# Kernel optimization log

Hardware: AMD Instinct MI355X
Metric: run time of the kernel (lower is better)

## Reference

```python
import jax, jax.numpy as jnp
import numpy as np

T = 2048
HIDDEN = 4096
NQ = 32
NKV = 8
HD = 128
THETA = 10000.0


def setup_inputs() -> dict:
    key = jax.random.key(0)
    ks = jax.random.split(key, 5)
    s = 1.0 / np.sqrt(HIDDEN)
    return {
        "positions": jnp.arange(T, dtype=jnp.int32),
        "hidden_states": jax.random.normal(ks[0], (T, HIDDEN), dtype=jnp.float32),
        "wq": jax.random.normal(ks[1], (HIDDEN, NQ * HD), dtype=jnp.float32) * s,
        "wk": jax.random.normal(ks[2], (HIDDEN, NKV * HD), dtype=jnp.float32) * s,
        "wv": jax.random.normal(ks[3], (HIDDEN, NKV * HD), dtype=jnp.float32) * s,
        "wo": jax.random.normal(ks[4], (NQ * HD, HIDDEN), dtype=jnp.float32) * s,
    }


def _rope_neox(x, positions):
    # x: [T, H, HD]; neox style: split halves, rotate
    half = HD // 2
    inv_freq = 1.0 / (THETA ** (jnp.arange(0, half, dtype=jnp.float32) / half))
    ang = positions.astype(jnp.float32)[:, None] * inv_freq[None, :]  # [T, half]
    cos = jnp.cos(ang)[:, None, :]  # [T, 1, half]
    sin = jnp.sin(ang)[:, None, :]
    x1, x2 = x[..., :half], x[..., half:]
    return jnp.concatenate([x1 * cos - x2 * sin, x2 * cos + x1 * sin], axis=-1)


def reference(positions, hidden_states, wq, wk, wv, wo):
    scale = HD ** -0.5
    q = (hidden_states @ wq).reshape(T, NQ, HD)
    k = (hidden_states @ wk).reshape(T, NKV, HD)
    v = (hidden_states @ wv).reshape(T, NKV, HD)
    q = _rope_neox(q, positions)
    k = _rope_neox(k, positions)
    # GQA: repeat kv heads to match q heads
    group = NQ // NKV
    k_r = jnp.repeat(k, group, axis=1)  # [T, NQ, HD]
    v_r = jnp.repeat(v, group, axis=1)
    scores = jnp.einsum('qhd,khd->hqk', q, k_r) * scale  # [NQ, T, T]
    causal = positions[:, None] >= positions[None, :]  # [T, T]
    scores = jnp.where(causal[None, :, :], scores, -jnp.inf)
    probs = jax.nn.softmax(scores, axis=-1)
    attn = jnp.einsum('hqk,khd->qhd', probs, v_r).reshape(T, NQ * HD)
    return attn @ wo
```

## Files before the change

### kernel.cpp

```cpp
#include <hip/hip_runtime.h>

#define T_SEQ  2048
#define HID    4096
#define NQH    32
#define NKVH   8
#define HDIM   128

typedef float  f32x4  __attribute__((ext_vector_type(4)));
typedef __bf16 bf16x8 __attribute__((ext_vector_type(8)));

__device__ __forceinline__ float bf2f(unsigned short u) {
  union { unsigned int i; float f; } v; v.i = ((unsigned int)u) << 16; return v.f;
}
__device__ __forceinline__ unsigned short f2bf(float f) {
  union { float f; unsigned int i; } v; v.f = f;
  unsigned int r = v.i + 0x7fffu + ((v.i >> 16) & 1u);
  return (unsigned short)(r >> 16);
}

__device__ __forceinline__ f32x4 mfma_bf16(bf16x8 a, bf16x8 b, f32x4 c) {
  return __builtin_amdgcn_mfma_f32_16x16x32_bf16(a, b, c, 0, 0, 0);
}

#define GLOAD16(g, l)                                              \
  __builtin_amdgcn_global_load_lds(                                \
      (const __attribute__((address_space(1))) void*)(g),          \
      (__attribute__((address_space(3))) void*)(l), 16, 0, 0)

__global__ void prep_all(const float* __restrict__ hs, unsigned short* __restrict__ hb,
                         const float* __restrict__ wq, unsigned short* __restrict__ wqt,
                         const float* __restrict__ wk, const float* __restrict__ wv,
                         unsigned short* __restrict__ wkvt) {
  __shared__ float tile[64][65];
  const int b = blockIdx.x;
  if (b < 8192) {
    long long i = ((long long)b * 256 + threadIdx.x) * 4;
    float4 v = *(const float4*)(hs + i);
    union { unsigned short u[4]; uint2 p; } o;
    o.u[0] = f2bf(v.x); o.u[1] = f2bf(v.y); o.u[2] = f2bf(v.z); o.u[3] = f2bf(v.w);
    *(uint2*)(hb + i) = o.p;
    return;
  }
  const float* W;
  unsigned short* dst;
  int N, n0, k0;
  if (b < 12288) {
    int bid = b - 8192;  W = wq;  dst = wqt;  N = 4096;
    n0 = (bid & 63) * 64; k0 = (bid >> 6) * 64;
  } else if (b < 13312) {
    int bid = b - 12288; W = wk;  dst = wkvt; N = 1024;
    n0 = (bid & 15) * 64; k0 = (bid >> 4) * 64;
  } else {
    int bid = b - 13312; W = wv;  dst = wkvt + (size_t)1024 * HID; N = 1024;
    n0 = (bid & 15) * 64; k0 = (bid >> 4) * 64;
  }
  int tx = threadIdx.x & 15, ty = threadIdx.x >> 4;
#pragma unroll
  for (int i = 0; i < 4; i++) {
    int k = ty + 16 * i;
    float4 f = *(const float4*)(W + (long long)(k0 + k) * N + n0 + tx * 4);
    tile[tx * 4 + 0][k] = f.x;
    tile[tx * 4 + 1][k] = f.y;
    tile[tx * 4 + 2][k] = f.z;
    tile[tx * 4 + 3][k] = f.w;
  }
  __syncthreads();
#pragma unroll
  for (int i = 0; i < 4; i++) {
    int n = ty + 16 * i;
    union { unsigned short u[4]; uint2 p; } o;
    o.u[0] = f2bf(tile[n][tx * 4 + 0]);
    o.u[1] = f2bf(tile[n][tx * 4 + 1]);
    o.u[2] = f2bf(tile[n][tx * 4 + 2]);
    o.u[3] = f2bf(tile[n][tx * 4 + 3]);
    *(uint2*)(dst + (long long)(n0 + n) * HID + k0 + tx * 4) = o.p;
  }
}

__global__ void transpose_conv(const float* __restrict__ W,
                               unsigned short* __restrict__ Wt, int K, int N) {
  __shared__ float tile[64][65];
  int n0 = blockIdx.x * 64, k0 = blockIdx.y * 64;
  int tx = threadIdx.x & 15, ty = threadIdx.x >> 4;
#pragma unroll
  for (int i = 0; i < 4; i++) {
    int k = ty + 16 * i;
    float4 f = *(const float4*)(W + (long long)(k0 + k) * N + n0 + tx * 4);
    tile[tx * 4 + 0][k] = f.x;
    tile[tx * 4 + 1][k] = f.y;
    tile[tx * 4 + 2][k] = f.z;
    tile[tx * 4 + 3][k] = f.w;
  }
  __syncthreads();
#pragma unroll
  for (int i = 0; i < 4; i++) {
    int n = ty + 16 * i;
    union { unsigned short u[4]; uint2 p; } o;
    o.u[0] = f2bf(tile[n][tx * 4 + 0]);
    o.u[1] = f2bf(tile[n][tx * 4 + 1]);
    o.u[2] = f2bf(tile[n][tx * 4 + 2]);
    o.u[3] = f2bf(tile[n][tx * 4 + 3]);
    *(uint2*)(Wt + (long long)(n0 + n) * K + k0 + tx * 4) = o.p;
  }
}

template <int EPI>
__global__ __launch_bounds__(256) void gemm_bt(const unsigned short* __restrict__ A,
                                               const unsigned short* __restrict__ Bt,
                                               void* __restrict__ Cv,
                                               int M, int N, int K) {
  __shared__ unsigned short As[128 * 64];
  __shared__ unsigned short Bs[128 * 64];
  const int lin = blockIdx.y * gridDim.x + blockIdx.x;
  const int cpx = (gridDim.x * gridDim.y) >> 3;
  const int swz = (lin & 7) * cpx + (lin >> 3);
  const int bx = swz % gridDim.x, by = swz / gridDim.x;

  const int t = threadIdx.x;
  const int lane = t & 63, w = t >> 6;
  const int wr = w >> 1, wc = w & 1;
  const int l15 = lane & 15, lg = lane >> 4;
  const int m0 = by * 128, n0 = bx * 128;

  f32x4 acc[4][4];
#pragma unroll
  for (int i = 0; i < 4; i++)
#pragma unroll
    for (int j = 0; j < 4; j++) acc[i][j] = (f32x4){0.f, 0.f, 0.f, 0.f};

  for (int kt = 0; kt < K; kt += 64) {
    __syncthreads();
#pragma unroll
    for (int s = 0; s < 4; s++) {
      int c = t + s * 256;
      int row = c >> 3, sub = c & 7;
      GLOAD16(A + (long long)(m0 + row) * K + kt + ((sub ^ (row & 7)) * 8),
              (char*)As + (w * 64 + s * 256) * 16);
      GLOAD16(Bt + (long long)(n0 + row) * K + kt + ((sub ^ (row & 7)) * 8),
              (char*)Bs + (w * 64 + s * 256) * 16);
    }
    __syncthreads();

#pragma unroll
    for (int kk = 0; kk < 2; kk++) {
      bf16x8 af[4], bfr[4];
#pragma unroll
      for (int mi = 0; mi < 4; mi++) {
        int row = wr * 64 + mi * 16 + l15;
        af[mi] = *(const bf16x8*)(As + row * 64 + (((kk * 4 + lg) ^ (row & 7)) * 8));
      }
#pragma unroll
      for (int ni = 0; ni < 4; ni++) {
        int row = wc * 64 + ni * 16 + l15;
        bfr[ni] = *(const bf16x8*)(Bs + row * 64 + (((kk * 4 + lg) ^ (row & 7)) * 8));
      }
#pragma unroll
      for (int mi = 0; mi < 4; mi++)
#pragma unroll
        for (int ni = 0; ni < 4; ni++)
          acc[mi][ni] = mfma_bf16(af[mi], bfr[ni], acc[mi][ni]);
    }
  }

  const int row0 = m0 + wr * 64, col0 = n0 + wc * 64;
#pragma unroll
  for (int mi = 0; mi < 4; mi++)
#pragma unroll
    for (int ni = 0; ni < 4; ni++) {
      int rbase = row0 + mi * 16 + lg * 4;
      int col = col0 + ni * 16 + l15;
#pragma unroll
      for (int r = 0; r < 4; r++) {
        float v = acc[mi][ni][r];
        if (EPI == 0)
          ((unsigned short*)Cv)[(long long)(rbase + r) * N + col] = f2bf(v);
        else
          ((float*)Cv)[(long long)(rbase + r) * N + col] = v;
      }
    }
}

__global__ __launch_bounds__(256) void gemm_qkv(const unsigned short* __restrict__ A,
                                                const unsigned short* __restrict__ wqt,
                                                const unsigned short* __restrict__ wkvt,
                                                unsigned short* __restrict__ qb,
                                                unsigned short* __restrict__ kb,
                                                unsigned short* __restrict__ vtb) {
  __shared__ unsigned short S[2 * 128 * 64];
  unsigned short* As = S;
  unsigned short* Bs = S + 128 * 64;
  const int K = HID;

  const int lin = blockIdx.y * gridDim.x + blockIdx.x;
  const int cpx = (gridDim.x * gridDim.y) >> 3;
  const int swz = (lin & 7) * cpx + (lin >> 3);
  const int bx = swz % gridDim.x, by = swz / gridDim.x;

  const int t = threadIdx.x;
  const int lane = t & 63, w = t >> 6;
  const int wr = w >> 1, wc = w & 1;
  const int l15 = lane & 15, lg = lane >> 4;
  const int m0 = by * 128, n0 = bx * 128;

  const unsigned short* Brow = (n0 < 4096) ? (wqt + (long long)n0 * K)
                                           : (wkvt + (long long)(n0 - 4096) * K);

  f32x4 acc[4][4];
#pragma unroll
  for (int i = 0; i < 4; i++)
#pragma unroll
    for (int j = 0; j < 4; j++) acc[i][j] = (f32x4){0.f, 0.f, 0.f, 0.f};

  for (int kt = 0; kt < K; kt += 64) {
    __syncthreads();
#pragma unroll
    for (int s = 0; s < 4; s++) {
      int c = t + s * 256;
      int row = c >> 3, sub = c & 7;
      GLOAD16(A + (long long)(m0 + row) * K + kt + ((sub ^ (row & 7)) * 8),
              (char*)As + (w * 64 + s * 256) * 16);
      GLOAD16(Brow + (long long)row * K + kt + ((sub ^ (row & 7)) * 8),
              (char*)Bs + (w * 64 + s * 256) * 16);
    }
    __syncthreads();

#pragma unroll
    for (int kk = 0; kk < 2; kk++) {
      bf16x8 af[4], bfr[4];
#pragma unroll
      for (int mi = 0; mi < 4; mi++) {
        int row = wr * 64 + mi * 16 + l15;
        af[mi] = *(const bf16x8*)(As + row * 64 + (((kk * 4 + lg) ^ (row & 7)) * 8));
      }
#pragma unroll
      for (int ni = 0; ni < 4; ni++) {
        int row = wc * 64 + ni * 16 + l15;
        bfr[ni] = *(const bf16x8*)(Bs + row * 64 + (((kk * 4 + lg) ^ (row & 7)) * 8));
      }
#pragma unroll
      for (int mi = 0; mi < 4; mi++)
#pragma unroll
        for (int ni = 0; ni < 4; ni++)
          acc[mi][ni] = mfma_bf16(af[mi], bfr[ni], acc[mi][ni]);
    }
  }

  const int row0 = m0 + wr * 64;
  if (n0 < 4096) {
#pragma unroll
    for (int mi = 0; mi < 4; mi++)
#pragma unroll
      for (int ni = 0; ni < 4; ni++) {
        int rbase = row0 + mi * 16 + lg * 4;
        int col = n0 + wc * 64 + ni * 16 + l15;
#pragma unroll
        for (int r = 0; r < 4; r++)
          qb[(long long)(rbase + r) * 4096 + col] = f2bf(acc[mi][ni][r]);
      }
  } else if (n0 < 5120) {
#pragma unroll
    for (int mi = 0; mi < 4; mi++)
#pragma unroll
      for (int ni = 0; ni < 4; ni++) {
        int rbase = row0 + mi * 16 + lg * 4;
        int col = (n0 - 4096) + wc * 64 + ni * 16 + l15;
#pragma unroll
        for (int r = 0; r < 4; r++)
          kb[(long long)(rbase + r) * 1024 + col] = f2bf(acc[mi][ni][r]);
      }
  } else {
    __syncthreads();
    unsigned short* Tt = S;
#pragma unroll
    for (int mi = 0; mi < 4; mi++)
#pragma unroll
      for (int ni = 0; ni < 4; ni++) {
        int nloc = wc * 64 + ni * 16 + l15;
#pragma unroll
        for (int r = 0; r < 4; r++) {
          int mloc = wr * 64 + mi * 16 + lg * 4 + r;
          Tt[nloc * 128 + (mloc & 64) + ((mloc & 63) ^ ((nloc & 7) << 3))] =
              f2bf(acc[mi][ni][r]);
        }
      }
    __syncthreads();
    const int nloc = t >> 1;
    const int half = t & 1;
    const int d0 = n0 - 5120;
#pragma unroll
    for (int ci = 0; ci < 16; ci++) {
      uint2 v = *(const uint2*)(Tt + nloc * 128 + half * 64 +
                                (((ci >> 1) ^ (nloc & 7)) * 8 + (ci & 1) * 4));
      int nc = (ci >> 3) * 8 + 2 * (ci & 3) + ((ci >> 2) & 1);
      *(uint2*)(vtb + (long long)(d0 + nloc) * T_SEQ + m0 + half * 64 + nc * 4) = v;
    }
  }
}

__global__ void rope_all(unsigned short* __restrict__ qb,
                         unsigned short* __restrict__ kb,
                         const int* __restrict__ positions,
                         int* __restrict__ cnt) {
  if (blockIdx.x == 0 && threadIdx.x < 8) cnt[threadIdx.x] = 0;
  const int w = threadIdx.x >> 6, d = threadIdx.x & 63;
  const int gid = blockIdx.x * 4 + w;
  unsigned short* row;
  int t;
  bool isq;
  if (gid < T_SEQ * NQH) {
    int h = gid & (NQH - 1); t = gid >> 5;
    row = qb + (size_t)t * (NQH * HDIM) + (size_t)h * HDIM;
    isq = true;
  } else {
    int g = gid - T_SEQ * NQH;
    int h = g & (NKVH - 1); t = g >> 3;
    row = kb + (size_t)t * (NKVH * HDIM) + (size_t)h * HDIM;
    isq = false;
  }
  double inv = exp2(-(double)d * 0.20762050593046014);
  double ang = (double)positions[t] * inv;
  double c = cos(ang), s = sin(ang);
  if (isq) { c *= 0.12751744416986895; s *= 0.12751744416986895; }
  float x1 = bf2f(row[d]), x2 = bf2f(row[d + 64]);
  row[d]      = f2bf((float)((double)x1 * c - (double)x2 * s));
  row[d + 64] = f2bf((float)((double)x2 * c + (double)x1 * s));
}

__global__ __launch_bounds__(256) void attn_kernel(const unsigned short* __restrict__ qb,
                                                   const unsigned short* __restrict__ kb,
                                                   const unsigned short* __restrict__ vt,
                                                   unsigned short* __restrict__ ab,
                                                   int* __restrict__ cnt) {
  __shared__ unsigned short Ks[64 * 128];
  __shared__ unsigned short Vs[128 * 64];
  __shared__ int s_item;

  const int xcd = blockIdx.x & 7;
  const int kvh = xcd;
  const int t = threadIdx.x, lane = t & 63, w = t >> 6;
  const int l15 = lane & 15, lg = lane >> 4;

  for (;;) {
    __syncthreads();
    if (t == 0) s_item = atomicAdd(&cnt[xcd], 1);
    __syncthreads();
    const int item = s_item;
    if (item >= 128) break;
    const int j = 31 - (item >> 2);
    const int head = xcd * 4 + (item & 3);
    const int q0 = j * 64;

    bf16x8 qf[4];
#pragma unroll
    for (int kk = 0; kk < 4; kk++)
      qf[kk] = *(const bf16x8*)(qb + (long long)(q0 + w * 16 + l15) * (NQH * HDIM) +
                                head * HDIM + kk * 32 + lg * 8);

    f32x4 accO[8];
#pragma unroll
    for (int db = 0; db < 8; db++) accO[db] = (f32x4){0.f, 0.f, 0.f, 0.f};
    float mrun = -3e38f, lrun = 0.f;

    for (int kt = 0; kt <= j; kt++) {
      __syncthreads();
#pragma unroll
      for (int s = 0; s < 4; s++) {
        int c = t + s * 256;
        int row = c >> 4, chk = c & 15;
        GLOAD16(kb + (long long)(kt * 64 + row) * (NKVH * HDIM) + kvh * HDIM +
                    ((chk ^ (row & 7)) * 8),
                (char*)Ks + (w * 64 + s * 256) * 16);
      }
#pragma unroll
      for (int s = 0; s < 4; s++) {
        int c = t + s * 256;
        int row = c >> 3, chk = c & 7;
        GLOAD16(vt + (long long)(kvh * HDIM + row) * T_SEQ + kt * 64 +
                    ((chk ^ (row & 7)) * 8),
                (char*)Vs + (w * 64 + s * 256) * 16);
      }
      __syncthreads();

      f32x4 accS[4];
#pragma unroll
      for (int kc = 0; kc < 4; kc++) accS[kc] = (f32x4){0.f, 0.f, 0.f, 0.f};
      __builtin_amdgcn_s_setprio(1);
#pragma unroll
      for (int kk = 0; kk < 4; kk++)
#pragma unroll
        for (int kc = 0; kc < 4; kc++) {
          int row = kc * 16 + l15;
          bf16x8 a = *(const bf16x8*)(Ks + row * 128 + (((kk * 4 + lg) ^ (l15 & 7)) * 8));
          accS[kc] = mfma_bf16(a, qf[kk], accS[kc]);
        }
      __builtin_amdgcn_s_setprio(0);

      float pm[4][4];
      if (kt == j) {
        const int qloc = w * 16 + l15;
#pragma unroll
        for (int kc = 0; kc < 4; kc++)
#pragma unroll
          for (int r = 0; r < 4; r++)
            pm[kc][r] = (kc * 16 + lg * 4 + r > qloc) ? -3e38f : accS[kc][r];
      } else {
#pragma unroll
        for (int kc = 0; kc < 4; kc++)
#pragma unroll
          for (int r = 0; r < 4; r++) pm[kc][r] = accS[kc][r];
      }

      float rm = pm[0][0];
#pragma unroll
      for (int kc = 0; kc < 4; kc++)
#pragma unroll
        for (int r = 0; r < 4; r++) rm = fmaxf(rm, pm[kc][r]);
      if (__any(rm > mrun + 8.f)) {
        rm = fmaxf(rm, __shfl_xor(rm, 16, 64));
        rm = fmaxf(rm, __shfl_xor(rm, 32, 64));
        float mn = fmaxf(mrun, rm);
        float corr = exp2f(mrun - mn);
        mrun = mn;
        lrun *= corr;
        float cO[4];
#pragma unroll
        for (int r = 0; r < 4; r++) cO[r] = __shfl(corr, lg * 4 + r, 64);
#pragma unroll
        for (int db = 0; db < 8; db++)
#pragma unroll
          for (int r = 0; r < 4; r++) accO[db][r] *= cO[r];
      }

      float p[4][4];
#pragma unroll
      for (int kc = 0; kc < 4; kc++)
#pragma unroll
        for (int r = 0; r < 4; r++) {
          p[kc][r] = exp2f(pm[kc][r] - mrun);
          lrun += p[kc][r];
        }
      bf16x8 pa0, pa1;
#pragma unroll
      for (int jj = 0; jj < 8; jj++) {
        pa0[jj] = (__bf16)p[(jj >> 2)][jj & 3];
        pa1[jj] = (__bf16)p[2 + (jj >> 2)][jj & 3];
      }

      __builtin_amdgcn_s_setprio(1);
#pragma unroll
      for (int db = 0; db < 8; db++) {
        int vrow = db * 16 + l15;
        bf16x8 b = *(const bf16x8*)(Vs + vrow * 64 + ((lg ^ (vrow & 7)) * 8));
        accO[db] = mfma_bf16(pa0, b, accO[db]);
      }
#pragma unroll
      for (int db = 0; db < 8; db++) {
        int vrow = db * 16 + l15;
        bf16x8 b = *(const bf16x8*)(Vs + vrow * 64 + (((4 + lg) ^ (vrow & 7)) * 8));
        accO[db] = mfma_bf16(pa1, b, accO[db]);
      }
      __builtin_amdgcn_s_setprio(0);
    }

    lrun += __shfl_xor(lrun, 16, 64);
    lrun += __shfl_xor(lrun, 32, 64);
    float lO[4];
#pragma unroll
    for (int r = 0; r < 4; r++) lO[r] = __shfl(lrun, lg * 4 + r, 64);
#pragma unroll
    for (int db = 0; db < 8; db++)
#pragma unroll
      for (int r = 0; r < 4; r++) {
        int qr = q0 + w * 16 + lg * 4 + r;
        int col = head * HDIM + db * 16 + l15;
        ((__bf16*)ab)[(long long)qr * (NQH * HDIM) + col] = (__bf16)(accO[db][r] / lO[r]);
      }
  }
}

extern "C" void kernel_launch(void* const* d_in, const int* in_sizes, int n_in,
                              void* d_out, int out_size, void* d_ws, size_t ws_size,
                              hipStream_t stream) {
  const int*   positions = (const int*)d_in[0];
  const float* hs = (const float*)d_in[1];
  const float* wq = (const float*)d_in[2];
  const float* wk = (const float*)d_in[3];
  const float* wv = (const float*)d_in[4];
  const float* wo = (const float*)d_in[5];
  float* out = (float*)d_out;

  const size_t SZ_WQT = (size_t)HID * HID * 2;
  const size_t SZ_WKV = (size_t)2048 * HID * 2;
  const size_t SZ_HB  = (size_t)T_SEQ * HID * 2;
  const size_t SZ_QB  = (size_t)T_SEQ * NQH * HDIM * 2;
  const size_t SZ_KB  = (size_t)T_SEQ * NKVH * HDIM * 2;
  const size_t need = SZ_WQT + SZ_WKV + SZ_HB + SZ_QB + SZ_KB * 2 + 64;
  if (ws_size < need) return;

  char* p = (char*)d_ws;
  unsigned short* wqt  = (unsigned short*)p; p += SZ_WQT;
  unsigned short* wkvt = (unsigned short*)p; p += SZ_WKV;
  unsigned short* hb   = (unsigned short*)p; p += SZ_HB;
  unsigned short* qb   = (unsigned short*)p; p += SZ_QB;
  unsigned short* kb   = (unsigned short*)p; p += SZ_KB;
  unsigned short* vtb  = (unsigned short*)p; p += SZ_KB;
  int* cnt = (int*)p;
  unsigned short* ab   = hb;

  prep_all<<<14336, 256, 0, stream>>>(hs, hb, wq, wqt, wk, wv, wkvt);

  gemm_qkv<<<dim3(48, 16), 256, 0, stream>>>(hb, wqt, wkvt, qb, kb, vtb);

  rope_all<<<(T_SEQ * (NQH + NKVH)) / 4, 256, 0, stream>>>(qb, kb, positions, cnt);

  attn_kernel<<<512, 256, 0, stream>>>(qb, kb, vtb, ab, cnt);

  transpose_conv<<<dim3(HID / 64, (NQH * HDIM) / 64), 256, 0, stream>>>(wo, wqt, NQH * HDIM, HID);
  gemm_bt<2><<<dim3(HID / 128, T_SEQ / 128), 256, 0, stream>>>(ab, wqt, out, T_SEQ, HID, NQH * HDIM);
}
```

Baseline: 384.1 us.

## Split QKV GEMM into Q and KV tile types to balance grid

The fused QKV GEMM grid goes from 768 uniform 128x128 tiles to 1024 blocks. Blocks alternate in groups of eight between Q tiles (128x128) and K/V tiles that use a smaller 64x128 M tile. The aim is more blocks and a better wave fill across the GPU's compute units, with Q and KV work interleaved. The cost is that the smaller KV tiles reuse data less per block, and the V transpose epilogue is adapted to 64-row tiles.

New measurement: 384.4 us. Within noise of the previous version (+0.1%).

```diff
diff --git a/kernel.cpp b/kernel.cpp
--- a/kernel.cpp
+++ b/kernel.cpp
@@ -180,119 +180,168 @@
     }
 }
 
-__global__ __launch_bounds__(256) void gemm_qkv(const unsigned short* __restrict__ A,
-                                                const unsigned short* __restrict__ wqt,
-                                                const unsigned short* __restrict__ wkvt,
-                                                unsigned short* __restrict__ qb,
-                                                unsigned short* __restrict__ kb,
-                                                unsigned short* __restrict__ vtb) {
+__global__ __launch_bounds__(256) void gemm_qkv2(const unsigned short* __restrict__ A,
+                                                 const unsigned short* __restrict__ wqt,
+                                                 const unsigned short* __restrict__ wkvt,
+                                                 unsigned short* __restrict__ qb,
+                                                 unsigned short* __restrict__ kb,
+                                                 unsigned short* __restrict__ vtb) {
   __shared__ unsigned short S[2 * 128 * 64];
   unsigned short* As = S;
   unsigned short* Bs = S + 128 * 64;
   const int K = HID;
 
-  const int lin = blockIdx.y * gridDim.x + blockIdx.x;
-  const int cpx = (gridDim.x * gridDim.y) >> 3;
-  const int swz = (lin & 7) * cpx + (lin >> 3);
-  const int bx = swz % gridDim.x, by = swz / gridDim.x;
+  const int b = blockIdx.x;
+  const int type = (b >> 3) & 1;
+  const int id = ((b >> 4) << 3) | (b & 7);
 
   const int t = threadIdx.x;
   const int lane = t & 63, w = t >> 6;
   const int wr = w >> 1, wc = w & 1;
   const int l15 = lane & 15, lg = lane >> 4;
-  const int m0 = by * 128, n0 = bx * 128;
-
-  const unsigned short* Brow = (n0 < 4096) ? (wqt + (long long)n0 * K)
-                                           : (wkvt + (long long)(n0 - 4096) * K);
-
-  f32x4 acc[4][4];
-#pragma unroll
-  for (int i = 0; i < 4; i++)
-#pragma unroll
-    for (int j = 0; j < 4; j++) acc[i][j] = (f32x4){0.f, 0.f, 0.f, 0.f};
-
-  for (int kt = 0; kt < K; kt += 64) {
-    __syncthreads();
-#pragma unroll
-    for (int s = 0; s < 4; s++) {
-      int c = t + s * 256;
-      int row = c >> 3, sub = c & 7;
-      GLOAD16(A + (long long)(m0 + row) * K + kt + ((sub ^ (row & 7)) * 8),
-              (char*)As + (w * 64 + s * 256) * 16);
-      GLOAD16(Brow + (long long)row * K + kt + ((sub ^ (row & 7)) * 8),
-              (char*)Bs + (w * 64 + s * 256) * 16);
-    }
-    __syncthreads();
-
-#pragma unroll
-    for (int kk = 0; kk < 2; kk++) {
-      bf16x8 af[4], bfr[4];
-#pragma unroll
-      for (int mi = 0; mi < 4; mi++) {
-        int row = wr * 64 + mi * 16 + l15;
-        af[mi] = *(const bf16x8*)(As + row * 64 + (((kk * 4 + lg) ^ (row & 7)) * 8));
-      }
-#pragma unroll
-      for (int ni = 0; ni < 4; ni++) {
-        int row = wc * 64 + ni * 16 + l15;
-        bfr[ni] = *(const bf16x8*)(Bs + row * 64 + (((kk * 4 + lg) ^ (row & 7)) * 8));
-      }
-#pragma unroll
-      for (int mi = 0; mi < 4; mi++)
-#pragma unroll
-        for (int ni = 0; ni < 4; ni++)
-          acc[mi][ni] = mfma_bf16(af[mi], bfr[ni], acc[mi][ni]);
-    }
-  }
-
-  const int row0 = m0 + wr * 64;
-  if (n0 < 4096) {
+
+  if (type == 0) {
+    const int swz = (id & 7) * 64 + (id >> 3);
+    const int bx = swz & 31, by = swz >> 5;
+    const int m0 = by * 128, n0 = bx * 128;
+
+    f32x4 acc[4][4];
+#pragma unroll
+    for (int i = 0; i < 4; i++)
+#pragma unroll
+      for (int j = 0; j < 4; j++) acc[i][j] = (f32x4){0.f, 0.f, 0.f, 0.f};
+
+    for (int kt = 0; kt < K; kt += 64) {
+      __syncthreads();
+#pragma unroll
+      for (int s = 0; s < 4; s++) {
+        int c = t + s * 256;
+        int row = c >> 3, sub = c & 7;
+        GLOAD16(A + (long long)(m0 + row) * K + kt + ((sub ^ (row & 7)) * 8),
+                (char*)As + (w * 64 + s * 256) * 16);
+        GLOAD16(wqt + (long long)(n0 + row) * K + kt + ((sub ^ (row & 7)) * 8),
+                (char*)Bs + (w * 64 + s * 256) * 16);
+      }
+      __syncthreads();
+
+#pragma unroll
+      for (int kk = 0; kk < 2; kk++) {
+        bf16x8 af[4], bfr[4];
+#pragma unroll
+        for (int mi = 0; mi < 4; mi++) {
+          int row = wr * 64 + mi * 16 + l15;
+          af[mi] = *(const bf16x8*)(As + row * 64 + (((kk * 4 + lg) ^ (row & 7)) * 8));
+        }
+#pragma unroll
+        for (int ni = 0; ni < 4; ni++) {
+          int row = wc * 64 + ni * 16 + l15;
+          bfr[ni] = *(const bf16x8*)(Bs + row * 64 + (((kk * 4 + lg) ^ (row & 7)) * 8));
+        }
+#pragma unroll
+        for (int mi = 0; mi < 4; mi++)
+#pragma unroll
+          for (int ni = 0; ni < 4; ni++)
+            acc[mi][ni] = mfma_bf16(af[mi], bfr[ni], acc[mi][ni]);
+      }
+    }
+
+    const int row0 = m0 + wr * 64, col0 = n0 + wc * 64;
 #pragma unroll
     for (int mi = 0; mi < 4; mi++)
 #pragma unroll
       for (int ni = 0; ni < 4; ni++) {
         int rbase = row0 + mi * 16 + lg * 4;
-        int col = n0 + wc * 64 + ni * 16 + l15;
+        int col = col0 + ni * 16 + l15;
 #pragma unroll
         for (int r = 0; r < 4; r++)
-          qb[(long long)(rbase + r) * 4096 + col] = f2bf(acc[mi][ni][r]);
-      }
-  } else if (n0 < 5120) {
-#pragma unroll
-    for (int mi = 0; mi < 4; mi++)
-#pragma unroll
-      for (int ni = 0; ni < 4; ni++) {
-        int rbase = row0 + mi * 16 + lg * 4;
-        int col = (n0 - 4096) + wc * 64 + ni * 16 + l15;
-#pragma unroll
-        for (int r = 0; r < 4; r++)
-          kb[(long long)(rbase + r) * 1024 + col] = f2bf(acc[mi][ni][r]);
+          qb[(long long)(rbase + r) * (NQH * HDIM) + col] = f2bf(acc[mi][ni][r]);
       }
   } else {
-    __syncthreads();
-    unsigned short* Tt = S;
-#pragma unroll
-    for (int mi = 0; mi < 4; mi++)
-#pragma unroll
-      for (int ni = 0; ni < 4; ni++) {
-        int nloc = wc * 64 + ni * 16 + l15;
-#pragma unroll
-        for (int r = 0; r < 4; r++) {
-          int mloc = wr * 64 + mi * 16 + lg * 4 + r;
-          Tt[nloc * 128 + (mloc & 64) + ((mloc & 63) ^ ((nloc & 7) << 3))] =
-              f2bf(acc[mi][ni][r]);
-        }
-      }
-    __syncthreads();
-    const int nloc = t >> 1;
-    const int half = t & 1;
-    const int d0 = n0 - 5120;
-#pragma unroll
-    for (int ci = 0; ci < 16; ci++) {
-      uint2 v = *(const uint2*)(Tt + nloc * 128 + half * 64 +
-                                (((ci >> 1) ^ (nloc & 7)) * 8 + (ci & 1) * 4));
-      int nc = (ci >> 3) * 8 + 2 * (ci & 3) + ((ci >> 2) & 1);
-      *(uint2*)(vtb + (long long)(d0 + nloc) * T_SEQ + m0 + half * 64 + nc * 4) = v;
+    const int swz = (id & 7) * 64 + (id >> 3);
+    const int bx = swz & 15, by = swz >> 4;
+    const int m0 = by * 64, n0 = bx * 128;
+
+    f32x4 acc[2][4];
+#pragma unroll
+    for (int i = 0; i < 2; i++)
+#pragma unroll
+      for (int j = 0; j < 4; j++) acc[i][j] = (f32x4){0.f, 0.f, 0.f, 0.f};
+
+    for (int kt = 0; kt < K; kt += 64) {
+      __syncthreads();
+#pragma unroll
+      for (int s = 0; s < 2; s++) {
+        int c = t + s * 256;
+        int row = c >> 3, sub = c & 7;
+        GLOAD16(A + (long long)(m0 + row) * K + kt + ((sub ^ (row & 7)) * 8),
+                (char*)As + (w * 64 + s * 256) * 16);
+      }
+#pragma unroll
+      for (int s = 0; s < 4; s++) {
+        int c = t + s * 256;
+        int row = c >> 3, sub = c & 7;
+        GLOAD16(wkvt + (long long)(n0 + row) * K + kt + ((sub ^ (row & 7)) * 8),
+                (char*)Bs + (w * 64 + s * 256) * 16);
+      }
+      __syncthreads();
+
+#pragma unroll
+      for (int kk = 0; kk < 2; kk++) {
+        bf16x8 af[2], bfr[4];
+#pragma unroll
+        for (int mi = 0; mi < 2; mi++) {
+          int row = wr * 32 + mi * 16 + l15;
+          af[mi] = *(const bf16x8*)(As + row * 64 + (((kk * 4 + lg) ^ (row & 7)) * 8));
+        }
+#pragma unroll
+        for (int ni = 0; ni < 4; ni++) {
+          int row = wc * 64 + ni * 16 + l15;
+          bfr[ni] = *(const bf16x8*)(Bs + row * 64 + (((kk * 4 + lg) ^ (row & 7)) * 8));
+        }
+#pragma unroll
+        for (int mi = 0; mi < 2; mi++)
+#pragma unroll
+          for (int ni = 0; ni < 4; ni++)
+            acc[mi][ni] = mfma_bf16(af[mi], bfr[ni], acc[mi][ni]);
+      }
+    }
+
+    const int row0 = m0 + wr * 32, col0 = n0 + wc * 64;
+    if (n0 < 1024) {
+#pragma unroll
+      for (int mi = 0; mi < 2; mi++)
+#pragma unroll
+        for (int ni = 0; ni < 4; ni++) {
+          int rbase = row0 + mi * 16 + lg * 4;
+          int col = col0 + ni * 16 + l15;
+#pragma unroll
+          for (int r = 0; r < 4; r++)
+            kb[(long long)(rbase + r) * 1024 + col] = f2bf(acc[mi][ni][r]);
+        }
+    } else {
+      __syncthreads();
+      unsigned short* Tt = S;
+#pragma unroll
+      for (int mi = 0; mi < 2; mi++)
+#pragma unroll
+        for (int ni = 0; ni < 4; ni++) {
+          int nloc = wc * 64 + ni * 16 + l15;
+#pragma unroll
+          for (int r = 0; r < 4; r++) {
+            int mloc = wr * 32 + mi * 16 + lg * 4 + r;
+            Tt[nloc * 64 + (mloc ^ ((nloc & 7) << 3))] = f2bf(acc[mi][ni][r]);
+          }
+        }
+      __syncthreads();
+      const int nloc = t >> 1;
+#pragma unroll
+      for (int cc = 0; cc < 8; cc++) {
+        int ci = (t & 1) * 8 + cc;
+        uint2 v = *(const uint2*)(Tt + nloc * 64 +
+                                  (((ci >> 1) ^ (nloc & 7)) * 8 + (ci & 1) * 4));
+        int nc = (ci >> 3) * 8 + 2 * (ci & 3) + ((ci >> 2) & 1);
+        *(uint2*)(vtb + (long long)(n0 - 1024 + nloc) * T_SEQ + m0 + nc * 4) = v;
+      }
     }
   }
 }
@@ -509,7 +558,7 @@
 
   prep_all<<<14336, 256, 0, stream>>>(hs, hb, wq, wqt, wk, wv, wkvt);
 
-  gemm_qkv<<<dim3(48, 16), 256, 0, stream>>>(hb, wqt, wkvt, qb, kb, vtb);
+  gemm_qkv2<<<1024, 256, 0, stream>>>(hb, wqt, wkvt, qb, kb, vtb);
 
   rope_all<<<(T_SEQ * (NQH + NKVH)) / 4, 256, 0, stream>>>(qb, kb, positions, cnt);
 
```

## Double-buffer attention K/V tiles and split QKV GEMM into Q and KV kernels

Applied to the files above, without the earlier changes.

The attention kernel now keeps two shared-memory buffers for K and V. It prefetches the next key tile while computing on the current one, so global loads overlap MFMA work instead of sitting behind a barrier. The fused QKV projection is replaced by the generic gemm_bt for Q plus a new 64x128-tile KV GEMM. The smaller KV tiles give more blocks for the narrow K/V output. In exchange, attention shared memory doubles, which may lower occupancy, and the extra launch adds a little overhead.

New measurement: 357.5 us (median of 2 runs). 1.07x faster.

```diff
diff --git a/kernel.cpp b/kernel.cpp
--- a/kernel.cpp
+++ b/kernel.cpp
@@ -180,56 +180,54 @@
     }
 }
 
-__global__ __launch_bounds__(256) void gemm_qkv(const unsigned short* __restrict__ A,
-                                                const unsigned short* __restrict__ wqt,
-                                                const unsigned short* __restrict__ wkvt,
-                                                unsigned short* __restrict__ qb,
-                                                unsigned short* __restrict__ kb,
-                                                unsigned short* __restrict__ vtb) {
-  __shared__ unsigned short S[2 * 128 * 64];
-  unsigned short* As = S;
-  unsigned short* Bs = S + 128 * 64;
-  const int K = HID;
-
+__global__ __launch_bounds__(256) void gemm_kv64(const unsigned short* __restrict__ A,
+                                                 const unsigned short* __restrict__ Bt,
+                                                 unsigned short* __restrict__ Ckv,
+                                                 unsigned short* __restrict__ Cvt) {
+  __shared__ unsigned short As[64 * 64];
+  __shared__ unsigned short Bs[128 * 64];
+  __shared__ unsigned short Tt[128 * 64];
   const int lin = blockIdx.y * gridDim.x + blockIdx.x;
-  const int cpx = (gridDim.x * gridDim.y) >> 3;
-  const int swz = (lin & 7) * cpx + (lin >> 3);
-  const int bx = swz % gridDim.x, by = swz / gridDim.x;
+  const int swz = (lin & 7) * 64 + (lin >> 3);
+  const int bx = swz & 15, by = swz >> 4;
 
   const int t = threadIdx.x;
   const int lane = t & 63, w = t >> 6;
   const int wr = w >> 1, wc = w & 1;
   const int l15 = lane & 15, lg = lane >> 4;
-  const int m0 = by * 128, n0 = bx * 128;
-
-  const unsigned short* Brow = (n0 < 4096) ? (wqt + (long long)n0 * K)
-                                           : (wkvt + (long long)(n0 - 4096) * K);
-
-  f32x4 acc[4][4];
-#pragma unroll
-  for (int i = 0; i < 4; i++)
+  const int m0 = by * 64, n0 = bx * 128;
+  const int K = HID;
+
+  f32x4 acc[2][4];
+#pragma unroll
+  for (int i = 0; i < 2; i++)
 #pragma unroll
     for (int j = 0; j < 4; j++) acc[i][j] = (f32x4){0.f, 0.f, 0.f, 0.f};
 
   for (int kt = 0; kt < K; kt += 64) {
     __syncthreads();
 #pragma unroll
-    for (int s = 0; s < 4; s++) {
+    for (int s = 0; s < 2; s++) {
       int c = t + s * 256;
       int row = c >> 3, sub = c & 7;
       GLOAD16(A + (long long)(m0 + row) * K + kt + ((sub ^ (row & 7)) * 8),
               (char*)As + (w * 64 + s * 256) * 16);
-      GLOAD16(Brow + (long long)row * K + kt + ((sub ^ (row & 7)) * 8),
+    }
+#pragma unroll
+    for (int s = 0; s < 4; s++) {
+      int c = t + s * 256;
+      int row = c >> 3, sub = c & 7;
+      GLOAD16(Bt + (long long)(n0 + row) * K + kt + ((sub ^ (row & 7)) * 8),
               (char*)Bs + (w * 64 + s * 256) * 16);
     }
     __syncthreads();
 
 #pragma unroll
     for (int kk = 0; kk < 2; kk++) {
-      bf16x8 af[4], bfr[4];
-#pragma unroll
-      for (int mi = 0; mi < 4; mi++) {
-        int row = wr * 64 + mi * 16 + l15;
+      bf16x8 af[2], bfr[4];
+#pragma unroll
+      for (int mi = 0; mi < 2; mi++) {
+        int row = wr * 32 + mi * 16 + l15;
         af[mi] = *(const bf16x8*)(As + row * 64 + (((kk * 4 + lg) ^ (row & 7)) * 8));
       }
 #pragma unroll
@@ -238,61 +236,46 @@
         bfr[ni] = *(const bf16x8*)(Bs + row * 64 + (((kk * 4 + lg) ^ (row & 7)) * 8));
       }
 #pragma unroll
-      for (int mi = 0; mi < 4; mi++)
+      for (int mi = 0; mi < 2; mi++)
 #pragma unroll
         for (int ni = 0; ni < 4; ni++)
           acc[mi][ni] = mfma_bf16(af[mi], bfr[ni], acc[mi][ni]);
     }
   }
 
-  const int row0 = m0 + wr * 64;
-  if (n0 < 4096) {
-#pragma unroll
-    for (int mi = 0; mi < 4; mi++)
+  const int row0 = m0 + wr * 32, col0 = n0 + wc * 64;
+  if (n0 < 1024) {
+#pragma unroll
+    for (int mi = 0; mi < 2; mi++)
 #pragma unroll
       for (int ni = 0; ni < 4; ni++) {
         int rbase = row0 + mi * 16 + lg * 4;
-        int col = n0 + wc * 64 + ni * 16 + l15;
+        int col = col0 + ni * 16 + l15;
 #pragma unroll
         for (int r = 0; r < 4; r++)
-          qb[(long long)(rbase + r) * 4096 + col] = f2bf(acc[mi][ni][r]);
-      }
-  } else if (n0 < 5120) {
-#pragma unroll
-    for (int mi = 0; mi < 4; mi++)
-#pragma unroll
-      for (int ni = 0; ni < 4; ni++) {
-        int rbase = row0 + mi * 16 + lg * 4;
-        int col = (n0 - 4096) + wc * 64 + ni * 16 + l15;
-#pragma unroll
-        for (int r = 0; r < 4; r++)
-          kb[(long long)(rbase + r) * 1024 + col] = f2bf(acc[mi][ni][r]);
+          Ckv[(long long)(rbase + r) * 1024 + col] = f2bf(acc[mi][ni][r]);
       }
   } else {
-    __syncthreads();
-    unsigned short* Tt = S;
-#pragma unroll
-    for (int mi = 0; mi < 4; mi++)
+#pragma unroll
+    for (int mi = 0; mi < 2; mi++)
 #pragma unroll
       for (int ni = 0; ni < 4; ni++) {
         int nloc = wc * 64 + ni * 16 + l15;
 #pragma unroll
         for (int r = 0; r < 4; r++) {
-          int mloc = wr * 64 + mi * 16 + lg * 4 + r;
-          Tt[nloc * 128 + (mloc & 64) + ((mloc & 63) ^ ((nloc & 7) << 3))] =
-              f2bf(acc[mi][ni][r]);
+          int mloc = wr * 32 + mi * 16 + lg * 4 + r;
+          Tt[nloc * 64 + (mloc ^ ((nloc & 7) << 3))] = f2bf(acc[mi][ni][r]);
         }
       }
     __syncthreads();
     const int nloc = t >> 1;
-    const int half = t & 1;
-    const int d0 = n0 - 5120;
-#pragma unroll
-    for (int ci = 0; ci < 16; ci++) {
-      uint2 v = *(const uint2*)(Tt + nloc * 128 + half * 64 +
+#pragma unroll
+    for (int cc = 0; cc < 8; cc++) {
+      int ci = (t & 1) * 8 + cc;
+      uint2 v = *(const uint2*)(Tt + nloc * 64 +
                                 (((ci >> 1) ^ (nloc & 7)) * 8 + (ci & 1) * 4));
       int nc = (ci >> 3) * 8 + 2 * (ci & 3) + ((ci >> 2) & 1);
-      *(uint2*)(vtb + (long long)(d0 + nloc) * T_SEQ + m0 + half * 64 + nc * 4) = v;
+      *(uint2*)(Cvt + (long long)(n0 - 1024 + nloc) * T_SEQ + m0 + nc * 4) = v;
     }
   }
 }
@@ -331,14 +314,33 @@
                                                    const unsigned short* __restrict__ vt,
                                                    unsigned short* __restrict__ ab,
                                                    int* __restrict__ cnt) {
-  __shared__ unsigned short Ks[64 * 128];
-  __shared__ unsigned short Vs[128 * 64];
+  __shared__ unsigned short Ks[2][64 * 128];
+  __shared__ unsigned short Vs[2][128 * 64];
   __shared__ int s_item;
 
   const int xcd = blockIdx.x & 7;
   const int kvh = xcd;
   const int t = threadIdx.x, lane = t & 63, w = t >> 6;
   const int l15 = lane & 15, lg = lane >> 4;
+
+  auto stage = [&](int kts, int bsel) {
+#pragma unroll
+    for (int s = 0; s < 4; s++) {
+      int c = t + s * 256;
+      int row = c >> 4, chk = c & 15;
+      GLOAD16(kb + (long long)(kts * 64 + row) * (NKVH * HDIM) + kvh * HDIM +
+                  ((chk ^ (row & 7)) * 8),
+              (char*)(&Ks[bsel][0]) + (w * 64 + s * 256) * 16);
+    }
+#pragma unroll
+    for (int s = 0; s < 4; s++) {
+      int c = t + s * 256;
+      int row = c >> 3, chk = c & 7;
+      GLOAD16(vt + (long long)(kvh * HDIM + row) * T_SEQ + kts * 64 +
+                  ((chk ^ (row & 7)) * 8),
+              (char*)(&Vs[bsel][0]) + (w * 64 + s * 256) * 16);
+    }
+  };
 
   for (;;) {
     __syncthreads();
@@ -361,25 +363,11 @@
     for (int db = 0; db < 8; db++) accO[db] = (f32x4){0.f, 0.f, 0.f, 0.f};
     float mrun = -3e38f, lrun = 0.f;
 
+    stage(0, 0);
     for (int kt = 0; kt <= j; kt++) {
+      const int cur = kt & 1;
       __syncthreads();
-#pragma unroll
-      for (int s = 0; s < 4; s++) {
-        int c = t + s * 256;
-        int row = c >> 4, chk = c & 15;
-        GLOAD16(kb + (long long)(kt * 64 + row) * (NKVH * HDIM) + kvh * HDIM +
-                    ((chk ^ (row & 7)) * 8),
-                (char*)Ks + (w * 64 + s * 256) * 16);
-      }
-#pragma unroll
-      for (int s = 0; s < 4; s++) {
-        int c = t + s * 256;
-        int row = c >> 3, chk = c & 7;
-        GLOAD16(vt + (long long)(kvh * HDIM + row) * T_SEQ + kt * 64 +
-                    ((chk ^ (row & 7)) * 8),
-                (char*)Vs + (w * 64 + s * 256) * 16);
-      }
-      __syncthreads();
+      if (kt < j) stage(kt + 1, cur ^ 1);
 
       f32x4 accS[4];
 #pragma unroll
@@ -390,7 +378,7 @@
 #pragma unroll
         for (int kc = 0; kc < 4; kc++) {
           int row = kc * 16 + l15;
-          bf16x8 a = *(const bf16x8*)(Ks + row * 128 + (((kk * 4 + lg) ^ (l15 & 7)) * 8));
+          bf16x8 a = *(const bf16x8*)(&Ks[cur][0] + row * 128 + (((kk * 4 + lg) ^ (l15 & 7)) * 8));
           accS[kc] = mfma_bf16(a, qf[kk], accS[kc]);
         }
       __builtin_amdgcn_s_setprio(0);
@@ -450,13 +438,13 @@
 #pragma unroll
       for (int db = 0; db < 8; db++) {
         int vrow = db * 16 + l15;
-        bf16x8 b = *(const bf16x8*)(Vs + vrow * 64 + ((lg ^ (vrow & 7)) * 8));
+        bf16x8 b = *(const bf16x8*)(&Vs[cur][0] + vrow * 64 + ((lg ^ (vrow & 7)) * 8));
         accO[db] = mfma_bf16(pa0, b, accO[db]);
       }
 #pragma unroll
       for (int db = 0; db < 8; db++) {
         int vrow = db * 16 + l15;
-        bf16x8 b = *(const bf16x8*)(Vs + vrow * 64 + (((4 + lg) ^ (vrow & 7)) * 8));
+        bf16x8 b = *(const bf16x8*)(&Vs[cur][0] + vrow * 64 + (((4 + lg) ^ (vrow & 7)) * 8));
         accO[db] = mfma_bf16(pa1, b, accO[db]);
       }
       __builtin_amdgcn_s_setprio(0);
@@ -509,7 +497,8 @@
 
   prep_all<<<14336, 256, 0, stream>>>(hs, hb, wq, wqt, wk, wv, wkvt);
 
-  gemm_qkv<<<dim3(48, 16), 256, 0, stream>>>(hb, wqt, wkvt, qb, kb, vtb);
+  gemm_bt<0><<<dim3((NQH * HDIM) / 128, T_SEQ / 128), 256, 0, stream>>>(hb, wqt, qb, T_SEQ, NQH * HDIM, HID);
+  gemm_kv64<<<dim3(16, 32), 256, 0, stream>>>(hb, wkvt, kb, vtb);
 
   rope_all<<<(T_SEQ * (NQH + NKVH)) / 4, 256, 0, stream>>>(qb, kb, positions, cnt);
 
```
